# Kernel tuning notes

Measured on AMD Instinct MI355X. Metric: run time of the kernel, lower is better.

## Reference

```python
import jax, jax.numpy as jnp
import numpy as np

B = 64            # batchSize
F_ENC = 2048      # encodedFeatureSize = 128 features * 16 bits
H = 8192          # hiddenLayerSize
C = 100           # numberOfClasses
K = 8             # numberOfSynapsesPerSegment
THR = K // 2      # segment activation threshold (majority of synapses active)
NSEG = 2          # numberOfSegmentsPerNeuron


def _make_synapse_matrix(key, n_neurons, prev_size):
    # exactly K random synapses per neuron, values +1/-1 with equal prob
    k_idx, k_val = jax.random.split(key)
    cols = jax.random.randint(k_idx, (n_neurons, K), 0, prev_size)
    vals = jnp.where(jax.random.bernoulli(k_val, 0.5, (n_neurons, K)), 1.0, -1.0).astype(jnp.float32)
    rows = jnp.arange(n_neurons)[:, None]
    W = jnp.zeros((n_neurons, prev_size), dtype=jnp.float32)
    return W.at[rows, cols].set(vals)


def setup_inputs() -> dict:
    key = jax.random.key(0)
    ks = jax.random.split(key, 16)
    # binary encoded input (thermometer/gray-coded bits); rand in [0,1), binarized in reference
    x = jax.random.uniform(ks[0], (B, F_ENC), dtype=jnp.float32)
    W0_s0 = _make_synapse_matrix(ks[1], H, F_ENC)
    W0_s1 = _make_synapse_matrix(ks[2], H, F_ENC)
    W1_s0 = _make_synapse_matrix(ks[3], H, H)
    W1_s1 = _make_synapse_matrix(ks[4], H, H)
    W2_s0 = _make_synapse_matrix(ks[5], H, H)
    W2_s1 = _make_synapse_matrix(ks[6], H, H)
    # trained (non-binary) output connection strengths, one matrix per hidden layer
    O0 = jax.random.uniform(ks[7], (H, C), dtype=jnp.float32)
    O1 = jax.random.uniform(ks[8], (H, C), dtype=jnp.float32)
    O2 = jax.random.uniform(ks[9], (H, C), dtype=jnp.float32)
    return {"x": x, "W0_s0": W0_s0, "W0_s1": W0_s1, "W1_s0": W1_s0, "W1_s1": W1_s1,
            "W2_s0": W2_s0, "W2_s1": W2_s1, "O0": O0, "O1": O1, "O2": O2}


def _layer(a, W_s0, W_s1):
    # per-segment integer-valued synaptic sums over binary activations; a neuron
    # fires if ANY segment reaches the activation threshold
    z0 = a @ W_s0.T  # [B, H]
    z1 = a @ W_s1.T
    fired = jnp.logical_or(z0 >= THR, z1 >= THR)
    return fired.astype(jnp.float32)


def reference(x, W0_s0, W0_s1, W1_s0, W1_s1, W2_s0, W2_s1, O0, O1, O2):
    a0 = (x > 0.5).astype(jnp.float32)          # encoded binary input bits [B, F_ENC]
    a1 = _layer(a0, W0_s0, W0_s1)               # [B, H]
    a2 = _layer(a1, W1_s0, W1_s1)               # [B, H]
    a3 = _layer(a2, W2_s0, W2_s1)               # [B, H]
    # class scores: sum of output connection strengths from all active hidden neurons
    logits = a1 @ O0 + a2 @ O1 + a3 @ O2        # [B, C]
    return logits
```

## Files before the change

kernel.cpp:

```cpp
#include <hip/hip_runtime.h>
#include <stdint.h>

#define BATCH 64
#define F_ENC 2048
#define HID 8192
#define NCLS 100
#define NMAT 6

typedef unsigned long long ull;
typedef uint32_t u32x4 __attribute__((ext_vector_type(4)));

__global__ void pack_kernel(const float* __restrict__ x, ull* __restrict__ A0,
                            float* __restrict__ out) {
  int c = blockIdx.x * blockDim.x + threadIdx.x;
  for (int i = c; i < BATCH * NCLS; i += F_ENC) out[i] = 0.f;
  if (c < F_ENC) {
    ull m = 0;
#pragma unroll
    for (int b = 0; b < BATCH; ++b)
      m |= (ull)(x[(size_t)b * F_ENC + c] > 0.5f) << b;
    A0[c] = m;
  }
}

__device__ __forceinline__ void scan_vec(u32x4 w, int vecIdx,
                                         unsigned* s_cnt, uint16_t* s_ent) {
  uint32_t vals[4] = {w[0], w[1], w[2], w[3]};
#pragma unroll
  for (int e = 0; e < 4; ++e) {
    uint32_t u = vals[e];
    if (u != 0u) {
      unsigned slot = atomicAdd(s_cnt, 1u);
      s_ent[slot & 15u] = (uint16_t)(((vecIdx << 2) + e) | ((u >> 31) << 15));
    }
  }
}

__global__ void __launch_bounds__(256) sparsify_kernel(
    const uint32_t* __restrict__ W0a, const uint32_t* __restrict__ W0b,
    const uint32_t* __restrict__ W1a, const uint32_t* __restrict__ W1b,
    const uint32_t* __restrict__ W2a, const uint32_t* __restrict__ W2b,
    uint16_t* __restrict__ entries) {
  int m = blockIdx.x >> 13;
  int r = blockIdx.x & (HID - 1);
  const uint32_t* Wbase;
  switch (m) {
    case 0: Wbase = W0a; break;
    case 1: Wbase = W0b; break;
    case 2: Wbase = W1a; break;
    case 3: Wbase = W1b; break;
    case 4: Wbase = W2a; break;
    default: Wbase = W2b; break;
  }
  const int cols = (m < 2) ? F_ENC : HID;
  const u32x4* row = (const u32x4*)(Wbase + (size_t)r * cols);

  __shared__ unsigned s_cnt;
  __shared__ uint16_t s_ent[16];
  if (threadIdx.x == 0) s_cnt = 0u;
  __syncthreads();

  if (cols == F_ENC) {
    u32x4 w0 = __builtin_nontemporal_load(row + threadIdx.x);
    u32x4 w1 = __builtin_nontemporal_load(row + threadIdx.x + 256);
    asm volatile("" ::: "memory");
    uint32_t any = w0[0] | w0[1] | w0[2] | w0[3] |
                   w1[0] | w1[1] | w1[2] | w1[3];
    if (any) {
      scan_vec(w0, threadIdx.x, &s_cnt, s_ent);
      scan_vec(w1, threadIdx.x + 256, &s_cnt, s_ent);
    }
  } else {
    u32x4 w[8];
#pragma unroll
    for (int e = 0; e < 8; ++e)
      w[e] = __builtin_nontemporal_load(row + threadIdx.x + (e << 8));
    asm volatile("" ::: "memory");
    uint32_t any = 0;
#pragma unroll
    for (int e = 0; e < 8; ++e) any |= w[e][0] | w[e][1] | w[e][2] | w[e][3];
    if (any) {
#pragma unroll
      for (int e = 0; e < 8; ++e)
        scan_vec(w[e], threadIdx.x + (e << 8), &s_cnt, s_ent);
    }
  }
  __syncthreads();
  if (threadIdx.x < 8) {
    unsigned cnt = s_cnt;
    uint16_t v = (threadIdx.x < cnt) ? s_ent[threadIdx.x] : (uint16_t)0xFFFF;
    entries[(size_t)blockIdx.x * 8 + threadIdx.x] = v;
  }
}

struct BS4 { ull p0, p1, p2, p3; };

__device__ __forceinline__ void bs_add(BS4& a, ull m) {
  ull c = m, t;
  t = a.p0 ^ c; c &= a.p0; a.p0 = t;
  t = a.p1 ^ c; c &= a.p1; a.p1 = t;
  t = a.p2 ^ c; c &= a.p2; a.p2 = t;
  a.p3 ^= c;
}

__device__ __forceinline__ ull bs_fired(const BS4& A, const BS4& Mn) {
  ull b0 = Mn.p0, b1 = Mn.p1;
  ull carry = Mn.p2;
  ull b2 = ~Mn.p2;
  ull b3 = Mn.p3 ^ carry;
  ull b4 = Mn.p3 & carry;
  ull res = 0, eq = ~0ull;
  eq &= ~b4;
  res |= eq & A.p3 & ~b3; eq &= ~(A.p3 ^ b3);
  res |= eq & A.p2 & ~b2; eq &= ~(A.p2 ^ b2);
  res |= eq & A.p1 & ~b1; eq &= ~(A.p1 ^ b1);
  res |= eq & A.p0 & ~b0; eq &= ~(A.p0 ^ b0);
  return res | eq;
}

__global__ void __launch_bounds__(256) layer_kernel(
    const uint16_t* __restrict__ ent0, const uint16_t* __restrict__ ent1,
    const ull* __restrict__ Aprev, ull* __restrict__ Anext) {
  int h = blockIdx.x * blockDim.x + threadIdx.x;
  if (h >= HID) return;
  uint4 p0 = ((const uint4*)ent0)[h];
  uint4 p1 = ((const uint4*)ent1)[h];
  uint32_t wd[8] = {p0.x, p0.y, p0.z, p0.w, p1.x, p1.y, p1.z, p1.w};
  uint16_t es[16];
#pragma unroll
  for (int i = 0; i < 8; ++i) {
    es[2 * i]     = (uint16_t)(wd[i] & 0xFFFFu);
    es[2 * i + 1] = (uint16_t)(wd[i] >> 16);
  }
  ull M[16];
#pragma unroll
  for (int i = 0; i < 16; ++i) {
    int idx = (es[i] == 0xFFFF) ? 0 : (es[i] & 0x1FFF);
    ull v = Aprev[idx];
    M[i] = (es[i] == 0xFFFF) ? 0ull : v;
  }
  ull f = 0;
#pragma unroll
  for (int s = 0; s < 2; ++s) {
    BS4 P{0, 0, 0, 0}, N{0, 0, 0, 0};
#pragma unroll
    for (int i = 0; i < 8; ++i) {
      uint16_t e = es[s * 8 + i];
      ull Mm = M[s * 8 + i];
      ull mp = (e & 0x8000) ? 0ull : Mm;
      ull mn = (e & 0x8000) ? Mm : 0ull;
      bs_add(P, mp);
      bs_add(N, mn);
    }
    f |= bs_fired(P, N);
  }
  Anext[h] = f;
}

__global__ void __launch_bounds__(128) logits_kernel(
    const ull* __restrict__ A1, const ull* __restrict__ A2,
    const ull* __restrict__ A3,
    const float* __restrict__ O0, const float* __restrict__ O1,
    const float* __restrict__ O2, float* __restrict__ out) {
  __shared__ float acc[BATCH * NCLS];
  for (int i = threadIdx.x; i < BATCH * NCLS; i += 128) acc[i] = 0.f;
  __syncthreads();
  const int j = threadIdx.x;
  const int h0 = blockIdx.x * 32;
  if (j < NCLS) {
    for (int k = 0; k < 32; ++k) {
      int h = h0 + k;
      ull m1 = A1[h], m2 = A2[h], m3 = A3[h];
      if (m1) {
        float o = O0[(size_t)h * NCLS + j];
        do { int b = __builtin_ctzll(m1); m1 &= m1 - 1; acc[b * NCLS + j] += o; } while (m1);
      }
      if (m2) {
        float o = O1[(size_t)h * NCLS + j];
        do { int b = __builtin_ctzll(m2); m2 &= m2 - 1; acc[b * NCLS + j] += o; } while (m2);
      }
      if (m3) {
        float o = O2[(size_t)h * NCLS + j];
        do { int b = __builtin_ctzll(m3); m3 &= m3 - 1; acc[b * NCLS + j] += o; } while (m3);
      }
    }
  }
  __syncthreads();
  for (int i = threadIdx.x; i < BATCH * NCLS; i += 128)
    atomicAdd(&out[i], acc[i]);
}

extern "C" void kernel_launch(void* const* d_in, const int* in_sizes, int n_in,
                              void* d_out, int out_size, void* d_ws, size_t ws_size,
                              hipStream_t stream) {
  const float*    x   = (const float*)d_in[0];
  const uint32_t* W0a = (const uint32_t*)d_in[1];
  const uint32_t* W0b = (const uint32_t*)d_in[2];
  const uint32_t* W1a = (const uint32_t*)d_in[3];
  const uint32_t* W1b = (const uint32_t*)d_in[4];
  const uint32_t* W2a = (const uint32_t*)d_in[5];
  const uint32_t* W2b = (const uint32_t*)d_in[6];
  const float*    O0  = (const float*)d_in[7];
  const float*    O1  = (const float*)d_in[8];
  const float*    O2  = (const float*)d_in[9];
  float* out = (float*)d_out;
  char*  ws  = (char*)d_ws;

  ull* A0 = (ull*)(ws);
  ull* A1 = (ull*)(ws + 16384);
  ull* A2 = (ull*)(ws + 16384 + 65536);
  ull* A3 = (ull*)(ws + 16384 + 2 * 65536);
  uint16_t* entries = (uint16_t*)(ws + 16384 + 3 * 65536);

  pack_kernel<<<8, 256, 0, stream>>>(x, A0, out);
  sparsify_kernel<<<NMAT * HID, 256, 0, stream>>>(W0a, W0b, W1a, W1b, W2a, W2b,
                                                  entries);
  layer_kernel<<<HID / 256, 256, 0, stream>>>(
      entries + (size_t)0 * HID * 8, entries + (size_t)1 * HID * 8, A0, A1);
  layer_kernel<<<HID / 256, 256, 0, stream>>>(
      entries + (size_t)2 * HID * 8, entries + (size_t)3 * HID * 8, A1, A2);
  layer_kernel<<<HID / 256, 256, 0, stream>>>(
      entries + (size_t)4 * HID * 8, entries + (size_t)5 * HID * 8, A2, A3);
  logits_kernel<<<HID / 32, 128, 0, stream>>>(A1, A2, A3, O0, O1, O2, out);
}
```

Measured before the change: 226.2 us.

## Fuse pack, three layers and logits into one cooperative kernel with grid sync

Replaces the pack kernel, three layer kernels and the logits kernel with a single cooperative launch of 256 blocks that separates the stages with grid-wide syncs. The aim is to remove four kernel launch gaps and their dependency stalls. The logits stage now uses 256 threads per block, splitting the batch into two 32-bit halves so each thread walks fewer set bits. The risk is that grid.sync is costly and that cooperative launch adds its own overhead; the sparsify kernel, which dominates the time, is unchanged.

```diff
diff --git a/kernel.cpp b/kernel.cpp
--- a/kernel.cpp
+++ b/kernel.cpp
@@ -1,5 +1,8 @@
 #include <hip/hip_runtime.h>
+#include <hip/hip_cooperative_groups.h>
 #include <stdint.h>
+
+namespace cg = cooperative_groups;
 
 #define BATCH 64
 #define F_ENC 2048
@@ -9,19 +12,6 @@
 
 typedef unsigned long long ull;
 typedef uint32_t u32x4 __attribute__((ext_vector_type(4)));
-
-__global__ void pack_kernel(const float* __restrict__ x, ull* __restrict__ A0,
-                            float* __restrict__ out) {
-  int c = blockIdx.x * blockDim.x + threadIdx.x;
-  for (int i = c; i < BATCH * NCLS; i += F_ENC) out[i] = 0.f;
-  if (c < F_ENC) {
-    ull m = 0;
-#pragma unroll
-    for (int b = 0; b < BATCH; ++b)
-      m |= (ull)(x[(size_t)b * F_ENC + c] > 0.5f) << b;
-    A0[c] = m;
-  }
-}
 
 __device__ __forceinline__ void scan_vec(u32x4 w, int vecIdx,
                                          unsigned* s_cnt, uint16_t* s_ent) {
@@ -118,11 +108,10 @@
   return res | eq;
 }
 
-__global__ void __launch_bounds__(256) layer_kernel(
-    const uint16_t* __restrict__ ent0, const uint16_t* __restrict__ ent1,
-    const ull* __restrict__ Aprev, ull* __restrict__ Anext) {
-  int h = blockIdx.x * blockDim.x + threadIdx.x;
-  if (h >= HID) return;
+__device__ __forceinline__ ull layer_fire(const uint16_t* __restrict__ ent0,
+                                          const uint16_t* __restrict__ ent1,
+                                          const ull* __restrict__ Aprev,
+                                          int h) {
   uint4 p0 = ((const uint4*)ent0)[h];
   uint4 p1 = ((const uint4*)ent1)[h];
   uint32_t wd[8] = {p0.x, p0.y, p0.z, p0.w, p1.x, p1.y, p1.z, p1.w};
@@ -154,55 +143,86 @@
     }
     f |= bs_fired(P, N);
   }
-  Anext[h] = f;
-}
-
-__global__ void __launch_bounds__(128) logits_kernel(
-    const ull* __restrict__ A1, const ull* __restrict__ A2,
-    const ull* __restrict__ A3,
+  return f;
+}
+
+__global__ void __launch_bounds__(256) tail_kernel(
+    const float* __restrict__ x, const uint16_t* __restrict__ entries,
+    ull* __restrict__ A0, ull* __restrict__ A1, ull* __restrict__ A2,
+    ull* __restrict__ A3,
     const float* __restrict__ O0, const float* __restrict__ O1,
     const float* __restrict__ O2, float* __restrict__ out) {
+  cg::grid_group grid = cg::this_grid();
+  const int tid = blockIdx.x * 256 + threadIdx.x;
+
+  if (tid < BATCH * NCLS) out[tid] = 0.f;
+  if (tid < F_ENC) {
+    ull m = 0;
+#pragma unroll
+    for (int b = 0; b < BATCH; ++b)
+      m |= (ull)(x[(size_t)b * F_ENC + tid] > 0.5f) << b;
+    A0[tid] = m;
+  }
+  grid.sync();
+
+  if (tid < HID)
+    A1[tid] = layer_fire(entries + (size_t)0 * HID * 8,
+                         entries + (size_t)1 * HID * 8, A0, tid);
+  grid.sync();
+  if (tid < HID)
+    A2[tid] = layer_fire(entries + (size_t)2 * HID * 8,
+                         entries + (size_t)3 * HID * 8, A1, tid);
+  grid.sync();
+  if (tid < HID)
+    A3[tid] = layer_fire(entries + (size_t)4 * HID * 8,
+                         entries + (size_t)5 * HID * 8, A2, tid);
+  grid.sync();
+
   __shared__ float acc[BATCH * NCLS];
-  for (int i = threadIdx.x; i < BATCH * NCLS; i += 128) acc[i] = 0.f;
-  __syncthreads();
-  const int j = threadIdx.x;
+  for (int i = threadIdx.x; i < BATCH * NCLS; i += 256) acc[i] = 0.f;
+  __syncthreads();
+  const int half = threadIdx.x >> 7;
+  const int j = threadIdx.x & 127;
   const int h0 = blockIdx.x * 32;
   if (j < NCLS) {
+    const int bofs = half * 32;
     for (int k = 0; k < 32; ++k) {
       int h = h0 + k;
-      ull m1 = A1[h], m2 = A2[h], m3 = A3[h];
+      uint32_t m1 = (uint32_t)(A1[h] >> (half * 32));
+      uint32_t m2 = (uint32_t)(A2[h] >> (half * 32));
+      uint32_t m3 = (uint32_t)(A3[h] >> (half * 32));
       if (m1) {
         float o = O0[(size_t)h * NCLS + j];
-        do { int b = __builtin_ctzll(m1); m1 &= m1 - 1; acc[b * NCLS + j] += o; } while (m1);
+        do { int b = __builtin_ctz(m1); m1 &= m1 - 1; acc[(b + bofs) * NCLS + j] += o; } while (m1);
       }
       if (m2) {
         float o = O1[(size_t)h * NCLS + j];
-        do { int b = __builtin_ctzll(m2); m2 &= m2 - 1; acc[b * NCLS + j] += o; } while (m2);
+        do { int b = __builtin_ctz(m2); m2 &= m2 - 1; acc[(b + bofs) * NCLS + j] += o; } while (m2);
       }
       if (m3) {
         float o = O2[(size_t)h * NCLS + j];
-        do { int b = __builtin_ctzll(m3); m3 &= m3 - 1; acc[b * NCLS + j] += o; } while (m3);
+        do { int b = __builtin_ctz(m3); m3 &= m3 - 1; acc[(b + bofs) * NCLS + j] += o; } while (m3);
       }
     }
   }
   __syncthreads();
-  for (int i = threadIdx.x; i < BATCH * NCLS; i += 128)
+  for (int i = threadIdx.x; i < BATCH * NCLS; i += 256)
     atomicAdd(&out[i], acc[i]);
 }
 
 extern "C" void kernel_launch(void* const* d_in, const int* in_sizes, int n_in,
                               void* d_out, int out_size, void* d_ws, size_t ws_size,
                               hipStream_t stream) {
-  const float*    x   = (const float*)d_in[0];
+  const float* x   = (const float*)d_in[0];
   const uint32_t* W0a = (const uint32_t*)d_in[1];
   const uint32_t* W0b = (const uint32_t*)d_in[2];
   const uint32_t* W1a = (const uint32_t*)d_in[3];
   const uint32_t* W1b = (const uint32_t*)d_in[4];
   const uint32_t* W2a = (const uint32_t*)d_in[5];
   const uint32_t* W2b = (const uint32_t*)d_in[6];
-  const float*    O0  = (const float*)d_in[7];
-  const float*    O1  = (const float*)d_in[8];
-  const float*    O2  = (const float*)d_in[9];
+  const float* O0  = (const float*)d_in[7];
+  const float* O1  = (const float*)d_in[8];
+  const float* O2  = (const float*)d_in[9];
   float* out = (float*)d_out;
   char*  ws  = (char*)d_ws;
 
@@ -212,14 +232,12 @@
   ull* A3 = (ull*)(ws + 16384 + 2 * 65536);
   uint16_t* entries = (uint16_t*)(ws + 16384 + 3 * 65536);
 
-  pack_kernel<<<8, 256, 0, stream>>>(x, A0, out);
   sparsify_kernel<<<NMAT * HID, 256, 0, stream>>>(W0a, W0b, W1a, W1b, W2a, W2b,
                                                   entries);
-  layer_kernel<<<HID / 256, 256, 0, stream>>>(
-      entries + (size_t)0 * HID * 8, entries + (size_t)1 * HID * 8, A0, A1);
-  layer_kernel<<<HID / 256, 256, 0, stream>>>(
-      entries + (size_t)2 * HID * 8, entries + (size_t)3 * HID * 8, A1, A2);
-  layer_kernel<<<HID / 256, 256, 0, stream>>>(
-      entries + (size_t)4 * HID * 8, entries + (size_t)5 * HID * 8, A2, A3);
-  logits_kernel<<<HID / 32, 128, 0, stream>>>(A1, A2, A3, O0, O1, O2, out);
-}
+
+  void* args[] = {(void*)&x, (void*)&entries, (void*)&A0, (void*)&A1,
+                  (void*)&A2, (void*)&A3, (void*)&O0, (void*)&O1,
+                  (void*)&O2, (void*)&out};
+  hipLaunchCooperativeKernel((const void*)tail_kernel, dim3(256), dim3(256),
+                             args, 0, stream);
+}
```

Result: slower. 323.2 us (+42.9%).

## Fuse pack into sparsify, fold third layer into logits, split batch halves

Applied to the files above, without the earlier changes.

Input bit-packing and output zeroing move into extra blocks of the sparsify kernel, removing one launch. The third layer's firing computation is folded into the logits kernel, where each block computes its own 32 hidden neurons into shared memory, removing another launch and the A3 round trip. The logits kernel now uses 256 threads, with each half handling 32 batch rows via 32-bit masks, to shorten the serial ctz loops. Two launches and their gaps are saved at the cost of some redundant setup work per logits block.

```diff
diff --git a/kernel.cpp b/kernel.cpp
--- a/kernel.cpp
+++ b/kernel.cpp
@@ -6,22 +6,10 @@
 #define HID 8192
 #define NCLS 100
 #define NMAT 6
+#define EXTRA 9
 
 typedef unsigned long long ull;
 typedef uint32_t u32x4 __attribute__((ext_vector_type(4)));
-
-__global__ void pack_kernel(const float* __restrict__ x, ull* __restrict__ A0,
-                            float* __restrict__ out) {
-  int c = blockIdx.x * blockDim.x + threadIdx.x;
-  for (int i = c; i < BATCH * NCLS; i += F_ENC) out[i] = 0.f;
-  if (c < F_ENC) {
-    ull m = 0;
-#pragma unroll
-    for (int b = 0; b < BATCH; ++b)
-      m |= (ull)(x[(size_t)b * F_ENC + c] > 0.5f) << b;
-    A0[c] = m;
-  }
-}
 
 __device__ __forceinline__ void scan_vec(u32x4 w, int vecIdx,
                                          unsigned* s_cnt, uint16_t* s_ent) {
@@ -36,13 +24,28 @@
   }
 }
 
-__global__ void __launch_bounds__(256) sparsify_kernel(
+__global__ void __launch_bounds__(256) sparsify_pack_kernel(
     const uint32_t* __restrict__ W0a, const uint32_t* __restrict__ W0b,
     const uint32_t* __restrict__ W1a, const uint32_t* __restrict__ W1b,
     const uint32_t* __restrict__ W2a, const uint32_t* __restrict__ W2b,
-    uint16_t* __restrict__ entries) {
-  int m = blockIdx.x >> 13;
-  int r = blockIdx.x & (HID - 1);
+    const float* __restrict__ x, ull* __restrict__ A0,
+    float* __restrict__ out, uint16_t* __restrict__ entries) {
+  if (blockIdx.x < 8) {
+    int c = blockIdx.x * 256 + threadIdx.x;
+    ull m = 0;
+#pragma unroll
+    for (int b = 0; b < BATCH; ++b)
+      m |= (ull)(x[(size_t)b * F_ENC + c] > 0.5f) << b;
+    A0[c] = m;
+    return;
+  }
+  if (blockIdx.x == 8) {
+    for (int i = threadIdx.x; i < BATCH * NCLS; i += 256) out[i] = 0.f;
+    return;
+  }
+  int blk = blockIdx.x - EXTRA;
+  int m = blk >> 13;
+  int r = blk & (HID - 1);
   const uint32_t* Wbase;
   switch (m) {
     case 0: Wbase = W0a; break;
@@ -89,7 +92,7 @@
   if (threadIdx.x < 8) {
     unsigned cnt = s_cnt;
     uint16_t v = (threadIdx.x < cnt) ? s_ent[threadIdx.x] : (uint16_t)0xFFFF;
-    entries[(size_t)blockIdx.x * 8 + threadIdx.x] = v;
+    entries[(size_t)blk * 8 + threadIdx.x] = v;
   }
 }
 
@@ -118,11 +121,10 @@
   return res | eq;
 }
 
-__global__ void __launch_bounds__(256) layer_kernel(
-    const uint16_t* __restrict__ ent0, const uint16_t* __restrict__ ent1,
-    const ull* __restrict__ Aprev, ull* __restrict__ Anext) {
-  int h = blockIdx.x * blockDim.x + threadIdx.x;
-  if (h >= HID) return;
+__device__ __forceinline__ ull layer_fire(const uint16_t* __restrict__ ent0,
+                                          const uint16_t* __restrict__ ent1,
+                                          const ull* __restrict__ Aprev,
+                                          int h) {
   uint4 p0 = ((const uint4*)ent0)[h];
   uint4 p1 = ((const uint4*)ent1)[h];
   uint32_t wd[8] = {p0.x, p0.y, p0.z, p0.w, p1.x, p1.y, p1.z, p1.w};
@@ -154,39 +156,55 @@
     }
     f |= bs_fired(P, N);
   }
-  Anext[h] = f;
-}
-
-__global__ void __launch_bounds__(128) logits_kernel(
+  return f;
+}
+
+__global__ void __launch_bounds__(256) layer_kernel(
+    const uint16_t* __restrict__ ent0, const uint16_t* __restrict__ ent1,
+    const ull* __restrict__ Aprev, ull* __restrict__ Anext) {
+  int h = blockIdx.x * blockDim.x + threadIdx.x;
+  if (h >= HID) return;
+  Anext[h] = layer_fire(ent0, ent1, Aprev, h);
+}
+
+__global__ void __launch_bounds__(256) logits_kernel(
+    const uint16_t* __restrict__ ent4, const uint16_t* __restrict__ ent5,
     const ull* __restrict__ A1, const ull* __restrict__ A2,
-    const ull* __restrict__ A3,
     const float* __restrict__ O0, const float* __restrict__ O1,
     const float* __restrict__ O2, float* __restrict__ out) {
   __shared__ float acc[BATCH * NCLS];
-  for (int i = threadIdx.x; i < BATCH * NCLS; i += 128) acc[i] = 0.f;
-  __syncthreads();
-  const int j = threadIdx.x;
+  __shared__ ull sA3[32];
   const int h0 = blockIdx.x * 32;
+  if (threadIdx.x < 32)
+    sA3[threadIdx.x] = layer_fire(ent4, ent5, A2, h0 + threadIdx.x);
+  for (int i = threadIdx.x; i < BATCH * NCLS; i += 256) acc[i] = 0.f;
+  __syncthreads();
+  const int half = threadIdx.x >> 7;
+  const int j = threadIdx.x & 127;
   if (j < NCLS) {
+    const int bofs = half * 32;
+    const int sh = half * 32;
     for (int k = 0; k < 32; ++k) {
       int h = h0 + k;
-      ull m1 = A1[h], m2 = A2[h], m3 = A3[h];
+      uint32_t m1 = (uint32_t)(A1[h] >> sh);
+      uint32_t m2 = (uint32_t)(A2[h] >> sh);
+      uint32_t m3 = (uint32_t)(sA3[k] >> sh);
       if (m1) {
         float o = O0[(size_t)h * NCLS + j];
-        do { int b = __builtin_ctzll(m1); m1 &= m1 - 1; acc[b * NCLS + j] += o; } while (m1);
+        do { int b = __builtin_ctz(m1); m1 &= m1 - 1; acc[(b + bofs) * NCLS + j] += o; } while (m1);
       }
       if (m2) {
         float o = O1[(size_t)h * NCLS + j];
-        do { int b = __builtin_ctzll(m2); m2 &= m2 - 1; acc[b * NCLS + j] += o; } while (m2);
+        do { int b = __builtin_ctz(m2); m2 &= m2 - 1; acc[(b + bofs) * NCLS + j] += o; } while (m2);
       }
       if (m3) {
         float o = O2[(size_t)h * NCLS + j];
-        do { int b = __builtin_ctzll(m3); m3 &= m3 - 1; acc[b * NCLS + j] += o; } while (m3);
+        do { int b = __builtin_ctz(m3); m3 &= m3 - 1; acc[(b + bofs) * NCLS + j] += o; } while (m3);
       }
     }
   }
   __syncthreads();
-  for (int i = threadIdx.x; i < BATCH * NCLS; i += 128)
+  for (int i = threadIdx.x; i < BATCH * NCLS; i += 256)
     atomicAdd(&out[i], acc[i]);
 }
 
@@ -209,17 +227,15 @@
   ull* A0 = (ull*)(ws);
   ull* A1 = (ull*)(ws + 16384);
   ull* A2 = (ull*)(ws + 16384 + 65536);
-  ull* A3 = (ull*)(ws + 16384 + 2 * 65536);
-  uint16_t* entries = (uint16_t*)(ws + 16384 + 3 * 65536);
-
-  pack_kernel<<<8, 256, 0, stream>>>(x, A0, out);
-  sparsify_kernel<<<NMAT * HID, 256, 0, stream>>>(W0a, W0b, W1a, W1b, W2a, W2b,
-                                                  entries);
+  uint16_t* entries = (uint16_t*)(ws + 16384 + 2 * 65536);
+
+  sparsify_pack_kernel<<<EXTRA + NMAT * HID, 256, 0, stream>>>(
+      W0a, W0b, W1a, W1b, W2a, W2b, x, A0, out, entries);
   layer_kernel<<<HID / 256, 256, 0, stream>>>(
       entries + (size_t)0 * HID * 8, entries + (size_t)1 * HID * 8, A0, A1);
   layer_kernel<<<HID / 256, 256, 0, stream>>>(
       entries + (size_t)2 * HID * 8, entries + (size_t)3 * HID * 8, A1, A2);
-  layer_kernel<<<HID / 256, 256, 0, stream>>>(
-      entries + (size_t)4 * HID * 8, entries + (size_t)5 * HID * 8, A2, A3);
-  logits_kernel<<<HID / 32, 128, 0, stream>>>(A1, A2, A3, O0, O1, O2, out);
-}
+  logits_kernel<<<HID / 32, 256, 0, stream>>>(
+      entries + (size_t)4 * HID * 8, entries + (size_t)5 * HID * 8,
+      A1, A2, O0, O1, O2, out);
+}
```

New measurement: 213.6 us, median of 2. 1.06x faster.
